# Kernel optimization log

Hardware: AMD Instinct MI355X
Metric: run time of the kernel (lower is better)

## Reference

```python
import jax, jax.numpy as jnp
import numpy as np

N, B, H, D = 8, 4, 16, 64   # batch, beam, heads, head_dim
T, S, L = 16, 1024, 1024    # new tokens, prefix len, past len
E = H * D
SCALE = 1.0 / np.sqrt(D).astype(np.float32)


def setup_inputs() -> dict:
    key = jax.random.key(0)
    ks = jax.random.split(key, 10)
    wscale = 1.0 / np.sqrt(E).astype(np.float32)
    return {
        "hidden_states": jax.random.normal(ks[0], (N * B, T, E), jnp.float32),
        "attention_mask": jnp.zeros((N * B, 1, 1, S + L + T), jnp.float32),
        "rel_pos": jax.random.normal(ks[1], (N * B, H, T, S + L + T), jnp.float32) * 0.1,
        "past_prefix_key": jax.random.normal(ks[2], (N, H, S, D), jnp.float32),
        "past_prefix_value": jax.random.normal(ks[3], (N, H, S, D), jnp.float32),
        "past_key": jax.random.normal(ks[4], (N * B, H, L, D), jnp.float32),
        "past_value": jax.random.normal(ks[5], (N * B, H, L, D), jnp.float32),
        "Wq": jax.random.normal(ks[6], (E, E), jnp.float32) * wscale,
        "bq": jnp.zeros((E,), jnp.float32),
        "Wk": jax.random.normal(ks[7], (E, E), jnp.float32) * wscale,
        "bk": jnp.zeros((E,), jnp.float32),
        "Wv": jax.random.normal(ks[8], (E, E), jnp.float32) * wscale,
        "bv": jnp.zeros((E,), jnp.float32),
    }


def _heads(x):
    # (NB, T, E) -> (NB, H, T, D)
    nb, t, _ = x.shape
    return x.reshape(nb, t, H, D).transpose(0, 2, 1, 3)


def reference(hidden_states, attention_mask, rel_pos, past_prefix_key,
              past_prefix_value, past_key, past_value, Wq, bq, Wk, bk, Wv, bv):
    q = _heads(hidden_states @ Wq.T + bq)   # (NB,H,T,D)
    k = _heads(hidden_states @ Wk.T + bk)
    v = _heads(hidden_states @ Wv.T + bv)

    # prefix scores: batch-shared prefix KV, per-beam queries
    q5 = q.reshape(N, B, H, T, D)
    prefix_scores = jnp.einsum('bxhtd,bhsd->bxhts', q5, past_prefix_key)
    prefix_scores = prefix_scores.reshape(N * B, H, T, S) * SCALE

    key_layer = jnp.concatenate([past_key, k], axis=2)      # (NB,H,L+T,D)
    value_layer = jnp.concatenate([past_value, v], axis=2)
    scores = jnp.einsum('bhtd,bhsd->bhts', q, key_layer) * SCALE

    scores = jnp.concatenate([prefix_scores, scores], axis=-1)  # (NB,H,T,S+L+T)
    scores = scores + rel_pos + attention_mask
    probs = jax.nn.softmax(scores, axis=-1)

    prefix_probs = probs[..., :S]
    rest_probs = probs[..., S:]

    prefix_ctx = jnp.einsum('bxhts,bhsd->bxhtd',
                            prefix_probs.reshape(N, B, H, T, S),
                            past_prefix_value).reshape(N * B, H, T, D)
    ctx = prefix_ctx + jnp.einsum('bhts,bhsd->bhtd', rest_probs, value_layer)

    # (NB,H,T,D) -> (NB,T,E)
    return ctx.transpose(0, 2, 1, 3).reshape(N * B, T, E)
```

## Files before the change

### kernel.cpp

```cpp
#include <hip/hip_runtime.h>

#define NH 16
#define NT 16
#define DD 64
#define SS 1024
#define LL 1024
#define TOTK 2064
#define EE 1024
#define NWAVE 8

typedef __attribute__((ext_vector_type(8))) short bf16x8;
typedef __attribute__((ext_vector_type(4))) float f32x4;

__device__ __forceinline__ unsigned short f2bf(float x) {
  union { float f; unsigned u; } v; v.f = x;
  unsigned r = v.u + 0x7fffu + ((v.u >> 16) & 1u);
  return (unsigned short)(r >> 16);
}

__device__ __forceinline__ unsigned pkbf(float a, float b) {
  unsigned r;
  asm("v_cvt_pk_bf16_f32 %0, %1, %2" : "=v"(r) : "v"(a), "v"(b));
  return r;
}
union BF8 { unsigned u[4]; bf16x8 v; };

__device__ __forceinline__ void dma16(const void* g, void* l) {
  __builtin_amdgcn_global_load_lds(
      (const __attribute__((address_space(1))) unsigned int*)g,
      (__attribute__((address_space(3))) unsigned int*)l, 16, 0, 0);
}

__global__ __launch_bounds__(256)
void proj_kernel(const float* __restrict__ hidden,
                 const float* __restrict__ Wq, const float* __restrict__ bq,
                 const float* __restrict__ Wk, const float* __restrict__ bk,
                 const float* __restrict__ Wv, const float* __restrict__ bv,
                 unsigned short* __restrict__ qws,
                 float* __restrict__ kws, float* __restrict__ vws)
{
  __shared__ alignas(16) unsigned short As[64][72];
  __shared__ alignas(16) unsigned short Bs[64][72];
  const int mtile = blockIdx.x;
  const int ntile = blockIdx.y;
  const int mat = ntile >> 4;
  const int h = ntile & 15;
  const float* Wm = (mat == 0) ? Wq : (mat == 1 ? Wk : Wv);
  const float* bm = (mat == 0) ? bq : (mat == 1 ? bk : bv);
  const int tid = threadIdx.x;
  const int lane = tid & 63, w = tid >> 6;
  const int lr = lane & 15, lg = lane >> 4;
  const int m0 = mtile * 64;

  const f32x4 fz = {0.f, 0.f, 0.f, 0.f};
  f32x4 acc[4];
  #pragma unroll
  for (int j = 0; j < 4; ++j) acc[j] = fz;

  const int srow = tid >> 4, sc4 = tid & 15;
  float4 Ar[4], Br[4];
  #pragma unroll
  for (int it = 0; it < 4; ++it) {
    Ar[it] = *(const float4*)(hidden + (m0 + srow + it * 16) * EE + sc4 * 4);
    Br[it] = *(const float4*)(Wm + (h * 64 + srow + it * 16) * EE + sc4 * 4);
  }

  for (int k0 = 0; k0 < EE; k0 += 64) {
    __syncthreads();
    #pragma unroll
    for (int it = 0; it < 4; ++it) {
      int row = srow + it * 16;
      float4 a = Ar[it], b = Br[it];
      *(uint2*)(&As[row][sc4 * 4]) = make_uint2(pkbf(a.x, a.y), pkbf(a.z, a.w));
      *(uint2*)(&Bs[row][sc4 * 4]) = make_uint2(pkbf(b.x, b.y), pkbf(b.z, b.w));
    }
    __syncthreads();
    int kn = k0 + 64;
    if (kn < EE) {
      #pragma unroll
      for (int it = 0; it < 4; ++it) {
        Ar[it] = *(const float4*)(hidden + (m0 + srow + it * 16) * EE + kn + sc4 * 4);
        Br[it] = *(const float4*)(Wm + (h * 64 + srow + it * 16) * EE + kn + sc4 * 4);
      }
    }
    #pragma unroll
    for (int hh = 0; hh < 2; ++hh) {
      bf16x8 a = *(const bf16x8*)(&As[w * 16 + lr][hh * 32 + lg * 8]);
      #pragma unroll
      for (int dt = 0; dt < 4; ++dt) {
        bf16x8 b = *(const bf16x8*)(&Bs[dt * 16 + lr][hh * 32 + lg * 8]);
        acc[dt] = __builtin_amdgcn_mfma_f32_16x16x32_bf16(a, b, acc[dt], 0, 0, 0);
      }
    }
  }

  #pragma unroll
  for (int dt = 0; dt < 4; ++dt)
    #pragma unroll
    for (int r = 0; r < 4; ++r) {
      int Mrow = m0 + w * 16 + lg * 4 + r;
      int nb = Mrow >> 4, t = Mrow & 15;
      int d = dt * 16 + lr;
      float val = acc[dt][r] + bm[h * 64 + d];
      int oi = ((nb * NH + h) * NT + t) * DD + d;
      if (mat == 0) qws[oi] = f2bf(val);
      else if (mat == 1) kws[oi] = val;
      else vws[oi] = val;
    }
}

__global__ __launch_bounds__(512, 2)
void attn_kernel(const float* __restrict__ mask, const float* __restrict__ rel,
                 const float* __restrict__ ppk, const float* __restrict__ ppv,
                 const float* __restrict__ pk, const float* __restrict__ pv,
                 const unsigned short* __restrict__ qws,
                 const float* __restrict__ kws, const float* __restrict__ vws,
                 float* __restrict__ out)
{
  __shared__ __align__(16) float SB[2 * 128 * 64];
  __shared__ __align__(16) unsigned short Pb[NWAVE][16][40];

  const int wg = blockIdx.x;
  const int nb = wg >> 4, h = wg & 15;
  const int n = nb >> 2;
  const int tid = threadIdx.x;
  const int lane = tid & 63, w = tid >> 6;
  const int lr = lane & 15, lg = lane >> 4;

  const unsigned short* qbase = qws + ((nb * NH + h) * NT) * DD;
  bf16x8 aq0 = *(const bf16x8*)(qbase + lr * DD + lg * 8);
  bf16x8 aq1 = *(const bf16x8*)(qbase + lr * DD + lg * 8 + 32);

  const float* relbase = rel + ((nb * NH + h) * NT) * TOTK;
  const float* mbase = mask + nb * TOTK;

  const f32x4 fz = {0.f, 0.f, 0.f, 0.f};
  f32x4 ctx[4];
  float ls[4];
  #pragma unroll
  for (int dt = 0; dt < 4; ++dt) ctx[dt] = fz;
  #pragma unroll
  for (int r = 0; r < 4; ++r) ls[r] = 0.f;

  auto kstage = [&](int c, int buf) {
    const float* ks = (c < 8)  ? ppk + ((n * NH + h) * SS + c * 128) * DD
                    : (c < 16) ? pk + ((nb * NH + h) * LL + (c - 8) * 128) * DD
                               : kws + ((nb * NH + h) * NT) * DD;
    float* Kb = SB + buf * 128 * 64;
    #pragma unroll
    for (int q = 0; q < 4; ++q) {
      int Lrow = w * 16 + q * 4 + (lane >> 4);
      int colb = (lane & 15) * 16;
      int scolb = colb ^ ((Lrow & 7) << 4);
      int srow = (c == 16) ? (Lrow & 15) : Lrow;
      dma16((const char*)ks + srow * 256 + scolb, Kb + (w * 16 + q * 4) * 64);
    }
  };

  auto qk_sub = [&](const float* Kb, const float rr[4], float mv, int sub) {
    bf16x8 kbf[2];
    #pragma unroll
    for (int hh = 0; hh < 2; ++hh) {
      int c0 = (hh * 128 + lg * 32) ^ ((lr & 7) << 4);
      int c1 = (hh * 128 + lg * 32 + 16) ^ ((lr & 7) << 4);
      float4 v0 = *(const float4*)((const char*)Kb + (w * 16 + lr) * 256 + c0);
      float4 v1 = *(const float4*)((const char*)Kb + (w * 16 + lr) * 256 + c1);
      BF8 o;
      o.u[0] = pkbf(v0.x, v0.y); o.u[1] = pkbf(v0.z, v0.w);
      o.u[2] = pkbf(v1.x, v1.y); o.u[3] = pkbf(v1.z, v1.w);
      kbf[hh] = o.v;
    }
    f32x4 s = fz;
    s = __builtin_amdgcn_mfma_f32_16x16x32_bf16(aq0, kbf[0], s, 0, 0, 0);
    s = __builtin_amdgcn_mfma_f32_16x16x32_bf16(aq1, kbf[1], s, 0, 0, 0);
    #pragma unroll
    for (int r = 0; r < 4; ++r) {
      float p = __expf(s[r] * 0.125f + rr[r] + mv);
      ls[r] += p;
      Pb[w][lg * 4 + r][sub * 16 + lr] = f2bf(p);
    }
  };

  auto rel_load = [&](int cA, float (&rA)[4], float (&rB)[4], float& mA, float& mB) {
    int kbA = cA * 128 + w * 16, kbB = kbA + 128;
    #pragma unroll
    for (int r = 0; r < 4; ++r) {
      rA[r] = relbase[(lg * 4 + r) * TOTK + kbA + lr];
      rB[r] = relbase[(lg * 4 + r) * TOTK + kbB + lr];
    }
    mA = mbase[kbA + lr];
    mB = mbase[kbB + lr];
  };

  auto pair_iter = [&](int p, float (&rA)[4], float (&rB)[4], float& mA, float& mB,
                       float (&rAn)[4], float (&rBn)[4], float& mAn, float& mBn) {
    const int cA = 2 * p;

    __builtin_amdgcn_sched_barrier(0);
    asm volatile("s_waitcnt vmcnt(10)" ::: "memory");
    __builtin_amdgcn_sched_barrier(0);

    const float* vs = (p < 4) ? ppv + ((n * NH + h) * SS + cA * 128) * DD
                              : pv + ((nb * NH + h) * LL + (cA - 8) * 128) * DD;
    float vraw[32];
    #pragma unroll
    for (int dt = 0; dt < 4; ++dt)
      #pragma unroll
      for (int e = 0; e < 8; ++e) {
        int kslot = lg * 8 + e;
        int j = (kslot >> 4) * 128 + w * 16 + (kslot & 15);
        vraw[dt * 8 + e] = vs[j * DD + dt * 16 + lr];
      }
    __builtin_amdgcn_sched_barrier(0);

    qk_sub(SB, rA, mA, 0);
    qk_sub(SB + 128 * 64, rB, mB, 1);

    __builtin_amdgcn_sched_barrier(0);
    if (p < 7) {
      kstage(cA + 2, 0);
      kstage(cA + 3, 1);
      rel_load(cA + 2, rAn, rBn, mAn, mBn);
    } else {
      kstage(16, 0);
    }
    __builtin_amdgcn_sched_barrier(0);

    bf16x8 pa = *(const bf16x8*)(&Pb[w][lr][lg * 8]);
    #pragma unroll
    for (int dt = 0; dt < 4; ++dt) {
      BF8 o;
      #pragma unroll
      for (int q = 0; q < 4; ++q)
        o.u[q] = pkbf(vraw[dt * 8 + q * 2], vraw[dt * 8 + q * 2 + 1]);
      ctx[dt] = __builtin_amdgcn_mfma_f32_16x16x32_bf16(pa, o.v, ctx[dt], 0, 0, 0);
    }
  };

  kstage(0, 0);
  kstage(1, 1);
  float ra0[4], rb0[4], ma0, mb0, ra1[4], rb1[4], ma1, mb1;
  rel_load(0, ra0, rb0, ma0, mb0);
  ma1 = mb1 = 0.f; ra1[0]=ra1[1]=ra1[2]=ra1[3]=0.f; rb1[0]=rb1[1]=rb1[2]=rb1[3]=0.f;

  for (int p = 0; p < 8; p += 2) {
    pair_iter(p,     ra0, rb0, ma0, mb0, ra1, rb1, ma1, mb1);
    pair_iter(p + 1, ra1, rb1, ma1, mb1, ra0, rb0, ma0, mb0);
  }

  if (w == 0) {
    #pragma unroll
    for (int r = 0; r < 4; ++r) Pb[0][lg * 4 + r][16 + lr] = 0;
    const float* vs = vws + ((nb * NH + h) * NT) * DD;
    float vraw[32];
    #pragma unroll
    for (int dt = 0; dt < 4; ++dt)
      #pragma unroll
      for (int e = 0; e < 8; ++e) {
        int kslot = lg * 8 + e;
        vraw[dt * 8 + e] = (kslot < 16) ? vs[kslot * DD + dt * 16 + lr] : 0.f;
      }
    float rrT[4];
    #pragma unroll
    for (int r = 0; r < 4; ++r)
      rrT[r] = relbase[(lg * 4 + r) * TOTK + 2048 + lr];
    float mvT = mbase[2048 + lr];

    __builtin_amdgcn_sched_barrier(0);
    asm volatile("s_waitcnt vmcnt(0)" ::: "memory");
    __builtin_amdgcn_sched_barrier(0);

    qk_sub(SB, rrT, mvT, 0);

    bf16x8 pa = *(const bf16x8*)(&Pb[0][lr][lg * 8]);
    #pragma unroll
    for (int dt = 0; dt < 4; ++dt) {
      BF8 o;
      #pragma unroll
      for (int q = 0; q < 4; ++q)
        o.u[q] = pkbf(vraw[dt * 8 + q * 2], vraw[dt * 8 + q * 2 + 1]);
      ctx[dt] = __builtin_amdgcn_mfma_f32_16x16x32_bf16(pa, o.v, ctx[dt], 0, 0, 0);
    }
  }

  #pragma unroll
  for (int r = 0; r < 4; ++r) {
    #pragma unroll
    for (int o = 8; o >= 1; o >>= 1) ls[r] += __shfl_xor(ls[r], o, 16);
  }

  __syncthreads();
  float* mgc = SB;
  float* mgl = SB + NWAVE * 16 * 64;
  #pragma unroll
  for (int dt = 0; dt < 4; ++dt)
    #pragma unroll
    for (int r = 0; r < 4; ++r)
      mgc[(w * 16 + lg * 4 + r) * 64 + dt * 16 + lr] = ctx[dt][r];
  if (lr == 0) {
    #pragma unroll
    for (int r = 0; r < 4; ++r) mgl[w * 16 + lg * 4 + r] = ls[r];
  }
  __syncthreads();
  #pragma unroll
  for (int i = 0; i < 2; ++i) {
    int idx = i * 512 + tid;
    int t = idx >> 6, d = idx & 63;
    float num = 0.f, den = 0.f;
    #pragma unroll
    for (int ww = 0; ww < NWAVE; ++ww) {
      den += mgl[ww * 16 + t];
      num += mgc[(ww * 16 + t) * 64 + d];
    }
    out[((nb * NT + t) * NH + h) * DD + d] = num / den;
  }
}

extern "C" void kernel_launch(void* const* d_in, const int* in_sizes, int n_in,
                              void* d_out, int out_size, void* d_ws, size_t ws_size,
                              hipStream_t stream) {
  const float* hidden = (const float*)d_in[0];
  const float* mask   = (const float*)d_in[1];
  const float* rel    = (const float*)d_in[2];
  const float* ppk    = (const float*)d_in[3];
  const float* ppv    = (const float*)d_in[4];
  const float* pk     = (const float*)d_in[5];
  const float* pv     = (const float*)d_in[6];
  const float* Wq     = (const float*)d_in[7];
  const float* bq     = (const float*)d_in[8];
  const float* Wk     = (const float*)d_in[9];
  const float* bk     = (const float*)d_in[10];
  const float* Wv     = (const float*)d_in[11];
  const float* bv     = (const float*)d_in[12];
  float* out = (float*)d_out;

  unsigned short* qws = (unsigned short*)d_ws;
  float* kws = (float*)((char*)d_ws + (1u << 20));
  float* vws = (float*)((char*)d_ws + 3u * (1u << 20));

  proj_kernel<<<dim3(8, 48), 256, 0, stream>>>(hidden, Wq, bq, Wk, bk, Wv, bv,
                                               qws, kws, vws);
  attn_kernel<<<dim3(512), 512, 0, stream>>>(mask, rel, ppk, ppv, pk, pv,
                                             qws, kws, vws, out);
}
```

Measured before the change: 109.0 us.

## Split prefix attention into beam-shared kernel reusing prefix K/V across beams

Adds a separate prefix attention kernel where each block handles one batch, head and half of the prefix keys for all four beams. Each prefix K/V tile is loaded and converted to bf16 once instead of once per beam. It writes partial numerators and denominators to workspace, and the past-attention kernel, now covering only past and new keys, adds them in its final reduction. This cuts redundant prefix K/V traffic but adds a kernel launch, a workspace round trip, and higher register pressure from holding four beams' accumulators.

```diff
diff --git a/kernel.cpp b/kernel.cpp
--- a/kernel.cpp
+++ b/kernel.cpp
@@ -17,7 +17,6 @@
   unsigned r = v.u + 0x7fffu + ((v.u >> 16) & 1u);
   return (unsigned short)(r >> 16);
 }
-
 __device__ __forceinline__ unsigned pkbf(float a, float b) {
   unsigned r;
   asm("v_cvt_pk_bf16_f32 %0, %1, %2" : "=v"(r) : "v"(a), "v"(b));
@@ -110,49 +109,222 @@
 }
 
 __global__ __launch_bounds__(512, 2)
-void attn_kernel(const float* __restrict__ mask, const float* __restrict__ rel,
-                 const float* __restrict__ ppk, const float* __restrict__ ppv,
-                 const float* __restrict__ pk, const float* __restrict__ pv,
-                 const unsigned short* __restrict__ qws,
-                 const float* __restrict__ kws, const float* __restrict__ vws,
-                 float* __restrict__ out)
+void prefix_attn_kernel(const float* __restrict__ mask, const float* __restrict__ rel,
+                        const float* __restrict__ ppk, const float* __restrict__ ppv,
+                        const unsigned short* __restrict__ qws,
+                        float* __restrict__ pfn, float* __restrict__ pfd)
 {
   __shared__ __align__(16) float SB[2 * 128 * 64];
   __shared__ __align__(16) unsigned short Pb[NWAVE][16][40];
 
-  const int wg = blockIdx.x;
-  const int nb = wg >> 4, h = wg & 15;
-  const int n = nb >> 2;
+  const int bidx = blockIdx.x;
+  const int h = bidx & 15;
+  const int sn = bidx >> 4;
+  const int nn = sn & 7;
+  const int s = sn >> 3;
   const int tid = threadIdx.x;
   const int lane = tid & 63, w = tid >> 6;
   const int lr = lane & 15, lg = lane >> 4;
-
-  const unsigned short* qbase = qws + ((nb * NH + h) * NT) * DD;
-  bf16x8 aq0 = *(const bf16x8*)(qbase + lr * DD + lg * 8);
-  bf16x8 aq1 = *(const bf16x8*)(qbase + lr * DD + lg * 8 + 32);
-
-  const float* relbase = rel + ((nb * NH + h) * NT) * TOTK;
-  const float* mbase = mask + nb * TOTK;
+  const int key0 = s * 512;
+
+  bf16x8 aq[4][2];
+  #pragma unroll
+  for (int b = 0; b < 4; ++b) {
+    const unsigned short* qb = qws + (((nn * 4 + b) * NH + h) * NT) * DD;
+    aq[b][0] = *(const bf16x8*)(qb + lr * DD + lg * 8);
+    aq[b][1] = *(const bf16x8*)(qb + lr * DD + lg * 8 + 32);
+  }
 
   const f32x4 fz = {0.f, 0.f, 0.f, 0.f};
-  f32x4 ctx[4];
-  float ls[4];
-  #pragma unroll
-  for (int dt = 0; dt < 4; ++dt) ctx[dt] = fz;
-  #pragma unroll
-  for (int r = 0; r < 4; ++r) ls[r] = 0.f;
+  f32x4 ctx[4][4];
+  float ls[4][4];
+  #pragma unroll
+  for (int b = 0; b < 4; ++b)
+    #pragma unroll
+    for (int j = 0; j < 4; ++j) { ctx[b][j] = fz; ls[b][j] = 0.f; }
 
   auto kstage = [&](int c, int buf) {
-    const float* ks = (c < 8)  ? ppk + ((n * NH + h) * SS + c * 128) * DD
-                    : (c < 16) ? pk + ((nb * NH + h) * LL + (c - 8) * 128) * DD
-                               : kws + ((nb * NH + h) * NT) * DD;
+    const float* ks = ppk + ((nn * NH + h) * SS + key0 + c * 128) * DD;
     float* Kb = SB + buf * 128 * 64;
     #pragma unroll
     for (int q = 0; q < 4; ++q) {
       int Lrow = w * 16 + q * 4 + (lane >> 4);
       int colb = (lane & 15) * 16;
       int scolb = colb ^ ((Lrow & 7) << 4);
-      int srow = (c == 16) ? (Lrow & 15) : Lrow;
+      dma16((const char*)ks + Lrow * 256 + scolb, Kb + (w * 16 + q * 4) * 64);
+    }
+  };
+
+  kstage(0, 0);
+  kstage(1, 1);
+
+  #pragma unroll
+  for (int p = 0; p < 2; ++p) {
+    const int cA = 2 * p;
+    const int kbA = key0 + cA * 128 + w * 16;
+
+    const float* vs = ppv + ((nn * NH + h) * SS + key0 + cA * 128) * DD;
+    float vraw[32];
+    #pragma unroll
+    for (int dt = 0; dt < 4; ++dt)
+      #pragma unroll
+      for (int e = 0; e < 8; ++e) {
+        int kslot = lg * 8 + e;
+        int j = (kslot >> 4) * 128 + w * 16 + (kslot & 15);
+        vraw[dt * 8 + e] = vs[j * DD + dt * 16 + lr];
+      }
+
+    __builtin_amdgcn_sched_barrier(0);
+    asm volatile("s_waitcnt vmcnt(32)" ::: "memory");
+    __builtin_amdgcn_sched_barrier(0);
+
+    float rr[4][2][4]; float mk[4][2];
+    #pragma unroll
+    for (int b = 0; b < 4; ++b) {
+      const float* relb = rel + (((nn * 4 + b) * NH + h) * NT) * TOTK;
+      const float* mb = mask + (nn * 4 + b) * TOTK;
+      #pragma unroll
+      for (int r = 0; r < 4; ++r) {
+        rr[b][0][r] = relb[(lg * 4 + r) * TOTK + kbA + lr];
+        rr[b][1][r] = relb[(lg * 4 + r) * TOTK + kbA + 128 + lr];
+      }
+      mk[b][0] = mb[kbA + lr];
+      mk[b][1] = mb[kbA + 128 + lr];
+    }
+
+    bf16x8 kbf[2][2];
+    #pragma unroll
+    for (int sub = 0; sub < 2; ++sub) {
+      const char* Kb = (const char*)(SB + sub * 128 * 64);
+      #pragma unroll
+      for (int hh = 0; hh < 2; ++hh) {
+        int c0 = (hh * 128 + lg * 32) ^ ((lr & 7) << 4);
+        int c1 = (hh * 128 + lg * 32 + 16) ^ ((lr & 7) << 4);
+        float4 v0 = *(const float4*)(Kb + (w * 16 + lr) * 256 + c0);
+        float4 v1 = *(const float4*)(Kb + (w * 16 + lr) * 256 + c1);
+        BF8 o;
+        o.u[0] = pkbf(v0.x, v0.y); o.u[1] = pkbf(v0.z, v0.w);
+        o.u[2] = pkbf(v1.x, v1.y); o.u[3] = pkbf(v1.z, v1.w);
+        kbf[sub][hh] = o.v;
+      }
+    }
+
+    __builtin_amdgcn_sched_barrier(0);
+    if (p == 0) { kstage(2, 0); kstage(3, 1); }
+    __builtin_amdgcn_sched_barrier(0);
+
+    bf16x8 vb[4];
+    #pragma unroll
+    for (int dt = 0; dt < 4; ++dt) {
+      BF8 o;
+      #pragma unroll
+      for (int q = 0; q < 4; ++q)
+        o.u[q] = pkbf(vraw[dt * 8 + q * 2], vraw[dt * 8 + q * 2 + 1]);
+      vb[dt] = o.v;
+    }
+
+    #pragma unroll
+    for (int b = 0; b < 4; ++b) {
+      f32x4 sA = fz, sB = fz;
+      sA = __builtin_amdgcn_mfma_f32_16x16x32_bf16(aq[b][0], kbf[0][0], sA, 0, 0, 0);
+      sA = __builtin_amdgcn_mfma_f32_16x16x32_bf16(aq[b][1], kbf[0][1], sA, 0, 0, 0);
+      sB = __builtin_amdgcn_mfma_f32_16x16x32_bf16(aq[b][0], kbf[1][0], sB, 0, 0, 0);
+      sB = __builtin_amdgcn_mfma_f32_16x16x32_bf16(aq[b][1], kbf[1][1], sB, 0, 0, 0);
+      #pragma unroll
+      for (int r = 0; r < 4; ++r) {
+        float pA = __expf(sA[r] * 0.125f + rr[b][0][r] + mk[b][0]);
+        float pB = __expf(sB[r] * 0.125f + rr[b][1][r] + mk[b][1]);
+        ls[b][r] += pA + pB;
+        Pb[w][lg * 4 + r][lr] = f2bf(pA);
+        Pb[w][lg * 4 + r][16 + lr] = f2bf(pB);
+      }
+      bf16x8 pa = *(const bf16x8*)(&Pb[w][lr][lg * 8]);
+      #pragma unroll
+      for (int dt = 0; dt < 4; ++dt)
+        ctx[b][dt] = __builtin_amdgcn_mfma_f32_16x16x32_bf16(pa, vb[dt], ctx[b][dt], 0, 0, 0);
+    }
+  }
+
+  #pragma unroll
+  for (int b = 0; b < 4; ++b)
+    #pragma unroll
+    for (int r = 0; r < 4; ++r) {
+      #pragma unroll
+      for (int o = 8; o >= 1; o >>= 1) ls[b][r] += __shfl_xor(ls[b][r], o, 16);
+    }
+
+  float* mgc = SB;
+  float* mgl = SB + NWAVE * 16 * 64;
+  for (int b = 0; b < 4; ++b) {
+    __syncthreads();
+    #pragma unroll
+    for (int dt = 0; dt < 4; ++dt)
+      #pragma unroll
+      for (int r = 0; r < 4; ++r)
+        mgc[(w * 16 + lg * 4 + r) * 64 + dt * 16 + lr] = ctx[b][dt][r];
+    if (lr == 0) {
+      #pragma unroll
+      for (int r = 0; r < 4; ++r) mgl[w * 16 + lg * 4 + r] = ls[b][r];
+    }
+    __syncthreads();
+    #pragma unroll
+    for (int i = 0; i < 2; ++i) {
+      int idx = i * 512 + tid;
+      int t = idx >> 6, d = idx & 63;
+      float num = 0.f, den = 0.f;
+      #pragma unroll
+      for (int ww = 0; ww < NWAVE; ++ww) {
+        den += mgl[ww * 16 + t];
+        num += mgc[(ww * 16 + t) * 64 + d];
+      }
+      pfn[((sn * 16 + h) * 4 + b) * 1024 + t * 64 + d] = num;
+      if (d == 0) pfd[((sn * 16 + h) * 4 + b) * 16 + t] = den;
+    }
+  }
+}
+
+__global__ __launch_bounds__(512, 2)
+void past_attn_kernel(const float* __restrict__ mask, const float* __restrict__ rel,
+                      const float* __restrict__ pk, const float* __restrict__ pv,
+                      const unsigned short* __restrict__ qws,
+                      const float* __restrict__ kws, const float* __restrict__ vws,
+                      const float* __restrict__ pfn, const float* __restrict__ pfd,
+                      float* __restrict__ out)
+{
+  __shared__ __align__(16) float SB[2 * 128 * 64];
+  __shared__ __align__(16) unsigned short Pb[NWAVE][16][40];
+
+  const int wg = blockIdx.x;
+  const int nb = wg >> 4, h = wg & 15;
+  const int tid = threadIdx.x;
+  const int lane = tid & 63, w = tid >> 6;
+  const int lr = lane & 15, lg = lane >> 4;
+
+  const unsigned short* qbase = qws + ((nb * NH + h) * NT) * DD;
+  bf16x8 aq0 = *(const bf16x8*)(qbase + lr * DD + lg * 8);
+  bf16x8 aq1 = *(const bf16x8*)(qbase + lr * DD + lg * 8 + 32);
+
+  const float* relbase = rel + ((nb * NH + h) * NT) * TOTK;
+  const float* mbase = mask + nb * TOTK;
+
+  const f32x4 fz = {0.f, 0.f, 0.f, 0.f};
+  f32x4 ctx[4];
+  float ls[4];
+  #pragma unroll
+  for (int dt = 0; dt < 4; ++dt) ctx[dt] = fz;
+  #pragma unroll
+  for (int r = 0; r < 4; ++r) ls[r] = 0.f;
+
+  auto kstage = [&](int c, int buf) {
+    const float* ks = (c < 8) ? pk + ((nb * NH + h) * LL + c * 128) * DD
+                              : kws + ((nb * NH + h) * NT) * DD;
+    float* Kb = SB + buf * 128 * 64;
+    #pragma unroll
+    for (int q = 0; q < 4; ++q) {
+      int Lrow = w * 16 + q * 4 + (lane >> 4);
+      int colb = (lane & 15) * 16;
+      int scolb = colb ^ ((Lrow & 7) << 4);
+      int srow = (c == 8) ? (Lrow & 15) : Lrow;
       dma16((const char*)ks + srow * 256 + scolb, Kb + (w * 16 + q * 4) * 64);
     }
   };
@@ -182,7 +354,7 @@
   };
 
   auto rel_load = [&](int cA, float (&rA)[4], float (&rB)[4], float& mA, float& mB) {
-    int kbA = cA * 128 + w * 16, kbB = kbA + 128;
+    int kbA = SS + cA * 128 + w * 16, kbB = kbA + 128;
     #pragma unroll
     for (int r = 0; r < 4; ++r) {
       rA[r] = relbase[(lg * 4 + r) * TOTK + kbA + lr];
@@ -200,8 +372,7 @@
     asm volatile("s_waitcnt vmcnt(10)" ::: "memory");
     __builtin_amdgcn_sched_barrier(0);
 
-    const float* vs = (p < 4) ? ppv + ((n * NH + h) * SS + cA * 128) * DD
-                              : pv + ((nb * NH + h) * LL + (cA - 8) * 128) * DD;
+    const float* vs = pv + ((nb * NH + h) * LL + cA * 128) * DD;
     float vraw[32];
     #pragma unroll
     for (int dt = 0; dt < 4; ++dt)
@@ -217,12 +388,12 @@
     qk_sub(SB + 128 * 64, rB, mB, 1);
 
     __builtin_amdgcn_sched_barrier(0);
-    if (p < 7) {
+    if (p < 3) {
       kstage(cA + 2, 0);
       kstage(cA + 3, 1);
       rel_load(cA + 2, rAn, rBn, mAn, mBn);
     } else {
-      kstage(16, 0);
+      kstage(8, 0);
     }
     __builtin_amdgcn_sched_barrier(0);
 
@@ -243,7 +414,7 @@
   rel_load(0, ra0, rb0, ma0, mb0);
   ma1 = mb1 = 0.f; ra1[0]=ra1[1]=ra1[2]=ra1[3]=0.f; rb1[0]=rb1[1]=rb1[2]=rb1[3]=0.f;
 
-  for (int p = 0; p < 8; p += 2) {
+  for (int p = 0; p < 4; p += 2) {
     pair_iter(p,     ra0, rb0, ma0, mb0, ra1, rb1, ma1, mb1);
     pair_iter(p + 1, ra1, rb1, ma1, mb1, ra0, rb0, ma0, mb0);
   }
@@ -302,6 +473,7 @@
     for (int r = 0; r < 4; ++r) mgl[w * 16 + lg * 4 + r] = ls[r];
   }
   __syncthreads();
+  const int n = nb >> 2, b = nb & 3;
   #pragma unroll
   for (int i = 0; i < 2; ++i) {
     int idx = i * 512 + tid;
@@ -311,6 +483,12 @@
     for (int ww = 0; ww < NWAVE; ++ww) {
       den += mgl[ww * 16 + t];
       num += mgc[(ww * 16 + t) * 64 + d];
+    }
+    #pragma unroll
+    for (int sp = 0; sp < 2; ++sp) {
+      int pbase = (((sp * 8 + n) * 16 + h) * 4 + b);
+      num += pfn[pbase * 1024 + t * 64 + d];
+      den += pfd[pbase * 16 + t];
     }
     out[((nb * NT + t) * NH + h) * DD + d] = num / den;
   }
@@ -337,9 +515,13 @@
   unsigned short* qws = (unsigned short*)d_ws;
   float* kws = (float*)((char*)d_ws + (1u << 20));
   float* vws = (float*)((char*)d_ws + 3u * (1u << 20));
+  float* pfn = (float*)((char*)d_ws + 5u * (1u << 20));
+  float* pfd = (float*)((char*)d_ws + 9u * (1u << 20));
 
   proj_kernel<<<dim3(8, 48), 256, 0, stream>>>(hidden, Wq, bq, Wk, bk, Wv, bv,
                                                qws, kws, vws);
-  attn_kernel<<<dim3(512), 512, 0, stream>>>(mask, rel, ppk, ppv, pk, pv,
-                                             qws, kws, vws, out);
-}
+  prefix_attn_kernel<<<dim3(256), 512, 0, stream>>>(mask, rel, ppk, ppv,
+                                                    qws, pfn, pfd);
+  past_attn_kernel<<<dim3(512), 512, 0, stream>>>(mask, rel, pk, pv,
+                                                  qws, kws, vws, pfn, pfd, out);
+}
```

Measured after the change: 110.0 us. Within noise of the previous version (+0.9%).
